# Kernel tuning notes

Hardware: AMD Instinct MI355X
Metric: run time of the kernel (lower is better)

The kernel has to match this reference:

```python
import jax, jax.numpy as jnp
import numpy as np

# Static graph layout: B equal-size graphs so per-graph topk has a fixed size.
NUM_GRAPHS = 512
NODES_PER_GRAPH = 256
K_PER_GRAPH = 128  # ceil(0.5 * NODES_PER_GRAPH), ratio = 0.5
NUM_EDGES = 4_194_304  # avg degree 32
D_FEAT = 128
D_EDGE = 16


def setup_inputs() -> dict:
    key = jax.random.key(0)
    k1, k2, k3, k4, k5, k6 = jax.random.split(key, 6)
    N = NUM_GRAPHS * NODES_PER_GRAPH
    x = jax.random.normal(k1, (N, D_FEAT), dtype=jnp.float32)
    # Edges are sampled within a graph (realistic PyG batched-graph structure).
    g = jax.random.randint(k2, (NUM_EDGES,), 0, NUM_GRAPHS)
    src = g * NODES_PER_GRAPH + jax.random.randint(k3, (NUM_EDGES,), 0, NODES_PER_GRAPH)
    dst = g * NODES_PER_GRAPH + jax.random.randint(k4, (NUM_EDGES,), 0, NODES_PER_GRAPH)
    edge_index = jnp.stack([src, dst]).astype(jnp.int32)
    edge_attr = jax.random.normal(k5, (NUM_EDGES, D_EDGE), dtype=jnp.float32)
    batch = jnp.repeat(jnp.arange(NUM_GRAPHS, dtype=jnp.int32), NODES_PER_GRAPH)
    W = jax.random.normal(k6, (D_FEAT,), dtype=jnp.float32) / np.sqrt(D_FEAT)
    b = jnp.zeros((1,), dtype=jnp.float32)
    return {"x": x, "edge_index": edge_index, "edge_attr": edge_attr,
            "batch": batch, "W": W, "b": b}


def reference(x, edge_index, edge_attr, batch, W, b):
    N, D = x.shape
    B, n, k = NUM_GRAPHS, NODES_PER_GRAPH, K_PER_GRAPH
    K = B * k

    # --- SelectSparse: linear scoring (Linear(in_channels, 1)) ---
    scores = x @ W + b[0]                      # [N]
    # Per-graph top-k (batch is sorted with equal-size graphs -> reshape).
    top_vals, top_idx = jax.lax.top_k(scores.reshape(B, n), k)  # [B, k]
    perm = (top_idx + (jnp.arange(B) * n)[:, None]).reshape(-1)  # [K] global ids
    w = top_vals.reshape(-1)                   # scores[perm], descending per graph

    # --- gather + scale selected node features ---
    x_out = x[perm] * w[:, None]               # [K, D]

    # --- FilterEdges: keep edges with both endpoints selected, remap ids ---
    node_map = jnp.full((N,), -1, dtype=jnp.int32).at[perm].set(
        jnp.arange(K, dtype=jnp.int32))
    new_src = node_map[edge_index[0]]
    new_dst = node_map[edge_index[1]]
    mask = (new_src >= 0) & (new_dst >= 0)
    # Stable-compaction of kept edges to the front; tail padded with -1 / 0
    # (fixed output shape in lieu of torch's dynamic-shape edge filtering).
    order = jnp.argsort(jnp.logical_not(mask), stable=True)
    kept = mask[order]
    new_ei = jnp.stack([new_src[order], new_dst[order]])
    new_ei = jnp.where(kept[None, :], new_ei, -1)   # [2, E]
    new_attr = jnp.where(kept[:, None], edge_attr[order], 0.0)  # [E, D_EDGE]
    new_batch = batch[perm]                    # [K]

    return x_out, new_ei, new_attr, new_batch, perm, w
```

## Files before the change

kernel.cpp:

```cpp
#include <hip/hip_runtime.h>

#define NGRAPH 512
#define NPG    256
#define KPG    128
#define NN     (NGRAPH * NPG)
#define KK     (NGRAPH * KPG)
#define NE     4194304
#define DF     128
#define DE     16

#define SBLK   256
#define EPB    1024
#define NTILE  (NE / EPB)

#define OUT_X     0ull
#define OUT_EI    ((size_t)KK * DF)
#define OUT_ATTR  (OUT_EI + 2ull * NE)
#define OUT_BATCH (OUT_ATTR + (size_t)NE * DE)
#define OUT_PERM  (OUT_BATCH + KK)
#define OUT_W     (OUT_PERM + KK)

__global__ void score_kernel(const float* __restrict__ x,
                             const float* __restrict__ W,
                             const float* __restrict__ b,
                             float* __restrict__ scores) {
    int t = threadIdx.x;
    int l32 = t & 31;
    int node = blockIdx.x * 8 + (t >> 5);
    float4 xv = ((const float4*)(x + (size_t)node * DF))[l32];
    float4 wv = ((const float4*)W)[l32];
    float s = xv.x * wv.x + xv.y * wv.y + xv.z * wv.z + xv.w * wv.w;
    #pragma unroll
    for (int off = 16; off > 0; off >>= 1) s += __shfl_down(s, off, 32);
    if (l32 == 0) scores[node] = s + b[0];
}

__global__ void __launch_bounds__(NPG)
topk_gather_kernel(const float* __restrict__ scores,
                   const float* __restrict__ x,
                   int* __restrict__ node_map,
                   unsigned* __restrict__ nkbits,
                   float* __restrict__ out) {
    __shared__ float s[NPG];
    __shared__ int   sel[KPG];
    __shared__ float selw[KPG];
    int g = blockIdx.x, t = threadIdx.x;
    int wave = t >> 6, lane = t & 63;
    float my = scores[g * NPG + t];
    s[t] = my;
    __syncthreads();
    int rank = 0;
    #pragma unroll 8
    for (int j = 0; j < NPG; j++) {
        float o = s[j];
        rank += (o > my) || (o == my && j < t);
    }
    bool kept = rank < KPG;
    if (kept) {
        int node = g * NPG + t;
        int nid  = g * KPG + rank;
        node_map[node] = nid;
        sel[rank]  = t;
        selw[rank] = my;
        out[OUT_BATCH + nid] = (float)g;
        out[OUT_PERM + nid]  = (float)node;
        out[OUT_W + nid]     = my;
    }
    unsigned long long bal = __ballot(kept);
    if (lane == 0)  nkbits[g * 8 + wave * 2]     = (unsigned)bal;
    if (lane == 32) nkbits[g * 8 + wave * 2 + 1] = (unsigned)(bal >> 32);
    __syncthreads();
    int l32 = t & 31, rsub = t >> 5;
    #pragma unroll
    for (int it = 0; it < KPG / 8; it++) {
        int r = it * 8 + rsub;
        int node = g * NPG + sel[r];
        float wv = selw[r];
        float4 v = ((const float4*)(x + (size_t)node * DF))[l32];
        v.x *= wv; v.y *= wv; v.z *= wv; v.w *= wv;
        ((float4*)(out + OUT_X + ((size_t)g * KPG + r) * DF))[l32] = v;
    }
}

__global__ void __launch_bounds__(SBLK)
mapcount_kernel(const int* __restrict__ ei,
                const unsigned* __restrict__ nkbits,
                unsigned* __restrict__ bitmap,
                int* __restrict__ tilecounts) {
    int tile = blockIdx.x, t = threadIdx.x;
    int ebase = tile * EPB + t * 4;
    int4 sv = *(const int4*)(ei + ebase);
    int4 dv = *(const int4*)(ei + NE + ebase);
    #define KB(n) ((nkbits[(unsigned)(n) >> 5] >> ((unsigned)(n) & 31u)) & 1u)
    unsigned bits = (KB(sv.x) & KB(dv.x))
                  | ((KB(sv.y) & KB(dv.y)) << 1)
                  | ((KB(sv.z) & KB(dv.z)) << 2)
                  | ((KB(sv.w) & KB(dv.w)) << 3);
    #undef KB
    __shared__ unsigned nib[SBLK];
    nib[t] = bits;
    __syncthreads();
    if (t < 32) {
        unsigned w = 0;
        #pragma unroll
        for (int k = 0; k < 8; k++) w |= nib[t * 8 + k] << (4 * k);
        bitmap[tile * 32 + t] = w;
        int c = __popc(w);
        #pragma unroll
        for (int off = 16; off > 0; off >>= 1) c += __shfl_down(c, off, 64);
        if (t == 0) tilecounts[tile] = c;
    }
}

__global__ void __launch_bounds__(256)
scan_kernel(const int* __restrict__ tilecounts,
            int* __restrict__ tileoffs) {
    const int PER = NTILE / 256;
    int t = threadIdx.x;
    int base = t * PER;
    int s = 0;
    #pragma unroll
    for (int j = 0; j < PER; j++) s += tilecounts[base + j];
    __shared__ int ls[256];
    ls[t] = s;
    __syncthreads();
    for (int off = 1; off < 256; off <<= 1) {
        int v = (t >= off) ? ls[t - off] : 0;
        __syncthreads();
        ls[t] += v;
        __syncthreads();
    }
    int run = ls[t] - s;
    #pragma unroll
    for (int j = 0; j < PER; j++) {
        int c = tilecounts[base + j];
        tileoffs[base + j] = run;
        run += c;
    }
}

__global__ void __launch_bounds__(SBLK)
scatter_kernel(const int* __restrict__ ei,
               const float* __restrict__ eattr,
               const int* __restrict__ node_map,
               const unsigned* __restrict__ bitmap,
               const int* __restrict__ tileoffs,
               float* __restrict__ out) {
    int tile = blockIdx.x, t = threadIdx.x;
    int lane = t & 63;
    __shared__ unsigned bmw[32];
    __shared__ int wordpre[32];
    __shared__ int s_cnt;
    __shared__ unsigned pk[EPB];
    __shared__ unsigned short kl[EPB];

    if (t < 32) {
        unsigned w = bitmap[tile * 32 + t];
        bmw[t] = w;
        int c = __popc(w);
        int v = c;
        #pragma unroll
        for (int off = 1; off < 32; off <<= 1) {
            int u = __shfl_up(v, off, 64);
            if (lane >= off) v += u;
        }
        wordpre[t] = v - c;
        if (t == 31) s_cnt = v;
    }
    __syncthreads();
    int cnt = s_cnt;

    int el0 = t * 4;
    unsigned word = bmw[t >> 3];
    int bit0 = (t & 7) * 4;
    unsigned mybits = (word >> bit0) & 0xFu;
    if (mybits) {
        int pre = wordpre[t >> 3] + __popc(word & ((1u << bit0) - 1u));
        int4 sv = *(const int4*)(ei + tile * EPB + el0);
        int4 dv = *(const int4*)(ei + NE + tile * EPB + el0);
        int s4[4] = {sv.x, sv.y, sv.z, sv.w};
        int d4[4] = {dv.x, dv.y, dv.z, dv.w};
        #pragma unroll
        for (int j = 0; j < 4; j++) {
            if ((mybits >> j) & 1u) {
                unsigned ns = (unsigned)node_map[s4[j]];
                unsigned nd = (unsigned)node_map[d4[j]];
                pk[pre] = (ns << 16) | nd;
                kl[pre] = (unsigned short)(el0 + j);
                pre++;
            }
        }
    }
    __syncthreads();
    int excl = tileoffs[tile];

    for (int j = t; j < cnt; j += SBLK) {
        unsigned p = pk[j];
        out[OUT_EI + excl + j]      = (float)(p >> 16);
        out[OUT_EI + NE + excl + j] = (float)(p & 0xFFFFu);
    }
    int sub = t & 3;
    for (int j = t >> 2; j < cnt; j += SBLK / 4) {
        int el = kl[j];
        float4 v = ((const float4*)(eattr + ((size_t)tile * EPB + el) * DE))[sub];
        ((float4*)(out + OUT_ATTR + ((size_t)excl + j) * DE))[sub] = v;
    }
    int disc_excl = tile * EPB - excl;
    int disc = EPB - cnt;
    size_t tail_lo = (size_t)NE - disc_excl - disc;
    for (int i = t; i < disc; i += SBLK) {
        out[OUT_EI + tail_lo + i]      = -1.f;
        out[OUT_EI + NE + tail_lo + i] = -1.f;
    }
    float4* ap = (float4*)(out + OUT_ATTR);
    float4 z = make_float4(0.f, 0.f, 0.f, 0.f);
    for (int i = t; i < disc * 4; i += SBLK)
        ap[tail_lo * 4 + i] = z;
}

extern "C" void kernel_launch(void* const* d_in, const int* in_sizes, int n_in,
                              void* d_out, int out_size, void* d_ws, size_t ws_size,
                              hipStream_t stream) {
    const float* x     = (const float*)d_in[0];
    const int*   ei    = (const int*)d_in[1];
    const float* eattr = (const float*)d_in[2];
    const float* W     = (const float*)d_in[4];
    const float* b     = (const float*)d_in[5];
    float* out = (float*)d_out;

    float*    scores     = (float*)d_ws;
    int*      node_map   = (int*)(scores + NN);
    unsigned* nkbits     = (unsigned*)(node_map + NN);
    unsigned* bitmap     = nkbits + NN / 32;
    int*      tilecounts = (int*)(bitmap + NE / 32);
    int*      tileoffs   = tilecounts + NTILE;

    score_kernel      <<<NN / 8, 256, 0, stream>>>(x, W, b, scores);
    topk_gather_kernel<<<NGRAPH, NPG, 0, stream>>>(scores, x, node_map, nkbits, out);
    mapcount_kernel   <<<NTILE, SBLK, 0, stream>>>(ei, nkbits, bitmap, tilecounts);
    scan_kernel       <<<1, 256, 0, stream>>>(tilecounts, tileoffs);
    scatter_kernel    <<<NTILE, SBLK, 0, stream>>>(ei, eattr, node_map, bitmap, tileoffs, out);
}
```

Baseline: 157.3 us.

## Compact kept edges in map stage to avoid re-reading edge_index in scatter

The map stage now computes per-tile prefix offsets with wave scans, looks up remapped node ids, and stages packed (src,dst) ids and local edge indices to workspace. The scatter kernel then reads only the compact staged data instead of reloading edge_index, rebuilding the bitmap prefix and gathering node_map again. Scatter loads and stores also become nontemporal to reduce cache pollution on streaming output. This adds workspace writes and reads of the staged arrays in exchange.

```diff
diff --git a/kernel.cpp b/kernel.cpp
--- a/kernel.cpp
+++ b/kernel.cpp
@@ -12,6 +12,8 @@
 #define SBLK   256
 #define EPB    1024
 #define NTILE  (NE / EPB)
+
+typedef float vf4 __attribute__((ext_vector_type(4)));
 
 #define OUT_X     0ull
 #define OUT_EI    ((size_t)KK * DF)
@@ -83,11 +85,16 @@
 }
 
 __global__ void __launch_bounds__(SBLK)
-mapcount_kernel(const int* __restrict__ ei,
+mapstage_kernel(const int* __restrict__ ei,
+                const int* __restrict__ node_map,
                 const unsigned* __restrict__ nkbits,
-                unsigned* __restrict__ bitmap,
+                unsigned* __restrict__ pk_ws,
+                unsigned short* __restrict__ kl_ws,
                 int* __restrict__ tilecounts) {
     int tile = blockIdx.x, t = threadIdx.x;
+    int wave = t >> 6, lane = t & 63;
+    __shared__ int wtot[4];
+
     int ebase = tile * EPB + t * 4;
     int4 sv = *(const int4*)(ei + ebase);
     int4 dv = *(const int4*)(ei + NE + ebase);
@@ -97,19 +104,35 @@
                   | ((KB(sv.z) & KB(dv.z)) << 2)
                   | ((KB(sv.w) & KB(dv.w)) << 3);
     #undef KB
-    __shared__ unsigned nib[SBLK];
-    nib[t] = bits;
-    __syncthreads();
-    if (t < 32) {
-        unsigned w = 0;
+    int c = __popc(bits);
+    int inc = c;
+    #pragma unroll
+    for (int off = 1; off < 64; off <<= 1) {
+        int u = __shfl_up(inc, off, 64);
+        if (lane >= off) inc += u;
+    }
+    if (lane == 63) wtot[wave] = inc;
+    __syncthreads();
+    int wbase = 0;
+    #pragma unroll
+    for (int i = 0; i < 4; i++) if (i < wave) wbase += wtot[i];
+    int pre = wbase + inc - c;
+
+    if (bits) {
+        int s4[4] = {sv.x, sv.y, sv.z, sv.w};
+        int d4[4] = {dv.x, dv.y, dv.z, dv.w};
         #pragma unroll
-        for (int k = 0; k < 8; k++) w |= nib[t * 8 + k] << (4 * k);
-        bitmap[tile * 32 + t] = w;
-        int c = __popc(w);
-        #pragma unroll
-        for (int off = 16; off > 0; off >>= 1) c += __shfl_down(c, off, 64);
-        if (t == 0) tilecounts[tile] = c;
-    }
+        for (int j = 0; j < 4; j++) {
+            if ((bits >> j) & 1u) {
+                unsigned ns = (unsigned)node_map[s4[j]];
+                unsigned nd = (unsigned)node_map[d4[j]];
+                pk_ws[tile * EPB + pre] = (ns << 16) | nd;
+                kl_ws[tile * EPB + pre] = (unsigned short)(t * 4 + j);
+                pre++;
+            }
+        }
+    }
+    if (t == 0) tilecounts[tile] = wtot[0] + wtot[1] + wtot[2] + wtot[3];
 }
 
 __global__ void __launch_bounds__(256)
@@ -140,82 +163,40 @@
 }
 
 __global__ void __launch_bounds__(SBLK)
-scatter_kernel(const int* __restrict__ ei,
-               const float* __restrict__ eattr,
-               const int* __restrict__ node_map,
-               const unsigned* __restrict__ bitmap,
+scatter_kernel(const float* __restrict__ eattr,
+               const unsigned* __restrict__ pk_ws,
+               const unsigned short* __restrict__ kl_ws,
+               const int* __restrict__ tilecounts,
                const int* __restrict__ tileoffs,
                float* __restrict__ out) {
     int tile = blockIdx.x, t = threadIdx.x;
-    int lane = t & 63;
-    __shared__ unsigned bmw[32];
-    __shared__ int wordpre[32];
-    __shared__ int s_cnt;
-    __shared__ unsigned pk[EPB];
-    __shared__ unsigned short kl[EPB];
-
-    if (t < 32) {
-        unsigned w = bitmap[tile * 32 + t];
-        bmw[t] = w;
-        int c = __popc(w);
-        int v = c;
-        #pragma unroll
-        for (int off = 1; off < 32; off <<= 1) {
-            int u = __shfl_up(v, off, 64);
-            if (lane >= off) v += u;
-        }
-        wordpre[t] = v - c;
-        if (t == 31) s_cnt = v;
-    }
-    __syncthreads();
-    int cnt = s_cnt;
-
-    int el0 = t * 4;
-    unsigned word = bmw[t >> 3];
-    int bit0 = (t & 7) * 4;
-    unsigned mybits = (word >> bit0) & 0xFu;
-    if (mybits) {
-        int pre = wordpre[t >> 3] + __popc(word & ((1u << bit0) - 1u));
-        int4 sv = *(const int4*)(ei + tile * EPB + el0);
-        int4 dv = *(const int4*)(ei + NE + tile * EPB + el0);
-        int s4[4] = {sv.x, sv.y, sv.z, sv.w};
-        int d4[4] = {dv.x, dv.y, dv.z, dv.w};
-        #pragma unroll
-        for (int j = 0; j < 4; j++) {
-            if ((mybits >> j) & 1u) {
-                unsigned ns = (unsigned)node_map[s4[j]];
-                unsigned nd = (unsigned)node_map[d4[j]];
-                pk[pre] = (ns << 16) | nd;
-                kl[pre] = (unsigned short)(el0 + j);
-                pre++;
-            }
-        }
-    }
-    __syncthreads();
+    int cnt  = tilecounts[tile];
     int excl = tileoffs[tile];
 
     for (int j = t; j < cnt; j += SBLK) {
-        unsigned p = pk[j];
-        out[OUT_EI + excl + j]      = (float)(p >> 16);
-        out[OUT_EI + NE + excl + j] = (float)(p & 0xFFFFu);
+        unsigned p = pk_ws[tile * EPB + j];
+        __builtin_nontemporal_store((float)(p >> 16),     &out[OUT_EI + excl + j]);
+        __builtin_nontemporal_store((float)(p & 0xFFFFu), &out[OUT_EI + NE + excl + j]);
     }
     int sub = t & 3;
     for (int j = t >> 2; j < cnt; j += SBLK / 4) {
-        int el = kl[j];
-        float4 v = ((const float4*)(eattr + ((size_t)tile * EPB + el) * DE))[sub];
-        ((float4*)(out + OUT_ATTR + ((size_t)excl + j) * DE))[sub] = v;
+        int el = kl_ws[tile * EPB + j];
+        const vf4* sp = (const vf4*)(eattr + ((size_t)tile * EPB + el) * DE);
+        vf4 v = __builtin_nontemporal_load(sp + sub);
+        vf4* dp = (vf4*)(out + OUT_ATTR + ((size_t)excl + j) * DE);
+        __builtin_nontemporal_store(v, dp + sub);
     }
     int disc_excl = tile * EPB - excl;
     int disc = EPB - cnt;
     size_t tail_lo = (size_t)NE - disc_excl - disc;
     for (int i = t; i < disc; i += SBLK) {
-        out[OUT_EI + tail_lo + i]      = -1.f;
-        out[OUT_EI + NE + tail_lo + i] = -1.f;
-    }
-    float4* ap = (float4*)(out + OUT_ATTR);
-    float4 z = make_float4(0.f, 0.f, 0.f, 0.f);
+        __builtin_nontemporal_store(-1.f, &out[OUT_EI + tail_lo + i]);
+        __builtin_nontemporal_store(-1.f, &out[OUT_EI + NE + tail_lo + i]);
+    }
+    vf4* ap = (vf4*)(out + OUT_ATTR);
+    vf4 z = (vf4){0.f, 0.f, 0.f, 0.f};
     for (int i = t; i < disc * 4; i += SBLK)
-        ap[tail_lo * 4 + i] = z;
+        __builtin_nontemporal_store(z, &ap[tail_lo * 4 + i]);
 }
 
 extern "C" void kernel_launch(void* const* d_in, const int* in_sizes, int n_in,
@@ -228,16 +209,17 @@
     const float* b     = (const float*)d_in[5];
     float* out = (float*)d_out;
 
-    float*    scores     = (float*)d_ws;
-    int*      node_map   = (int*)(scores + NN);
-    unsigned* nkbits     = (unsigned*)(node_map + NN);
-    unsigned* bitmap     = nkbits + NN / 32;
-    int*      tilecounts = (int*)(bitmap + NE / 32);
-    int*      tileoffs   = tilecounts + NTILE;
+    float*          scores     = (float*)d_ws;
+    int*            node_map   = (int*)(scores + NN);
+    unsigned*       nkbits     = (unsigned*)(node_map + NN);
+    int*            tilecounts = (int*)(nkbits + NN / 32);
+    int*            tileoffs   = tilecounts + NTILE;
+    unsigned*       pk_ws      = (unsigned*)(tileoffs + NTILE);
+    unsigned short* kl_ws      = (unsigned short*)(pk_ws + NE);
 
     score_kernel      <<<NN / 8, 256, 0, stream>>>(x, W, b, scores);
     topk_gather_kernel<<<NGRAPH, NPG, 0, stream>>>(scores, x, node_map, nkbits, out);
-    mapcount_kernel   <<<NTILE, SBLK, 0, stream>>>(ei, nkbits, bitmap, tilecounts);
+    mapstage_kernel   <<<NTILE, SBLK, 0, stream>>>(ei, node_map, nkbits, pk_ws, kl_ws, tilecounts);
     scan_kernel       <<<1, 256, 0, stream>>>(tilecounts, tileoffs);
-    scatter_kernel    <<<NTILE, SBLK, 0, stream>>>(ei, eattr, node_map, bitmap, tileoffs, out);
-}
+    scatter_kernel    <<<NTILE, SBLK, 0, stream>>>(eattr, pk_ws, kl_ws, tilecounts, tileoffs, out);
+}
```

New measurement: 151.8 us. -3.5%, faster.
